# Kernel optimization log

Measured on AMD Instinct MI355X. Metric: run time of the kernel, lower is better.

## Reference

```python
import jax, jax.numpy as jnp
import numpy as np

BN_EPS = 1e-5
LN_EPS = 1e-5

N_NODES = 50000
N_EDGES = 800000
D_IN = 128
D_HID = 512


def _batchnorm(h, gamma, beta):
    # training-mode BatchNorm1d: biased variance over the node/batch dim
    m = jnp.mean(h, axis=0)
    v = jnp.mean(jnp.square(h - m), axis=0)
    return (h - m) * jax.lax.rsqrt(v + BN_EPS) * gamma + beta


def setup_inputs() -> dict:
    key = jax.random.key(0)
    ks = jax.random.split(key, 8)
    x = jax.random.normal(ks[0], (N_NODES, D_IN), dtype=jnp.float32)
    edge_index = jax.random.randint(ks[1], (2, N_EDGES), 0, N_NODES, dtype=jnp.int64)
    s1 = 1.0 / np.sqrt(D_IN)
    s2 = 1.0 / np.sqrt(D_HID)
    W1 = jax.random.uniform(ks[2], (D_IN, D_HID), jnp.float32, -s1, s1)
    b1 = jax.random.uniform(ks[3], (D_HID,), jnp.float32, -s1, s1)
    W2 = jax.random.uniform(ks[4], (D_HID, D_IN), jnp.float32, -s2, s2)
    b2 = jax.random.uniform(ks[5], (D_IN,), jnp.float32, -s2, s2)
    return {
        "x": x,
        "edge_index": edge_index,
        "W1": W1, "b1": b1,
        "bn1_g": jnp.ones((D_HID,), jnp.float32), "bn1_b": jnp.zeros((D_HID,), jnp.float32),
        "W2": W2, "b2": b2,
        "bn2_g": jnp.ones((D_IN,), jnp.float32), "bn2_b": jnp.zeros((D_IN,), jnp.float32),
        "ln_g": jnp.ones((D_IN,), jnp.float32), "ln_b": jnp.zeros((D_IN,), jnp.float32),
    }


def reference(x, edge_index, W1, b1, bn1_g, bn1_b, W2, b2, bn2_g, bn2_b, ln_g, ln_b):
    n = x.shape[0]
    src = edge_index[0]
    dst = edge_index[1]
    # GIN aggregation: sum of neighbor (source) features at each destination node
    agg = jax.ops.segment_sum(x[src], dst, num_segments=n)  # [N, D_IN]
    h = x + agg  # (1 + eps) * x + agg, eps = 0
    # MLP: Linear -> BN -> ReLU -> Linear -> BN -> ReLU (final activation)
    h = jax.nn.relu(_batchnorm(h @ W1 + b1, bn1_g, bn1_b))  # [N, D_HID]
    h = jax.nn.relu(_batchnorm(h @ W2 + b2, bn2_g, bn2_b))  # [N, D_IN]
    # residual + LayerNorm (dropout p=0 -> identity)
    out = h + x
    m = jnp.mean(out, axis=-1, keepdims=True)
    v = jnp.mean(jnp.square(out - m), axis=-1, keepdims=True)
    out = (out - m) * jax.lax.rsqrt(v + LN_EPS) * ln_g + ln_b
    return out
```

## Files before the change

kernel.cpp:

```cpp
#include <hip/hip_runtime.h>
#include <stdint.h>

#define N_NODES 50000
#define N_EDGES 800000
#define D_IN    128
#define D_HID   512
#define NPAD    50048
#define NTILES  391
#define SCAN_NB 196
#define G_TILES 782
#define G_BLOCKS 256
#define H1_FULL_NEED 64797440LL
#define FILL_CH 2048
#define FILL_SUB ((N_EDGES + FILL_CH - 1) / FILL_CH)

typedef __attribute__((ext_vector_type(8))) short short8;
typedef __attribute__((ext_vector_type(4))) float f32x4;

__device__ __forceinline__ float bf2f(unsigned short u) {
    union { unsigned int i; float f; } v; v.i = ((unsigned int)u) << 16; return v.f;
}
__device__ __forceinline__ unsigned short f2bf(float f) {
    union { float f; unsigned int i; } v; v.f = f;
    unsigned int r = v.i + 0x7fffu + ((v.i >> 16) & 1u);
    return (unsigned short)(r >> 16);
}
__device__ __forceinline__ float loadP(const void* p, long i, int isf) {
    return isf ? ((const float*)p)[i] : bf2f(((const unsigned short*)p)[i]);
}

__global__ void k_init(const void* __restrict__ x, const int* __restrict__ ei,
                       float* __restrict__ stats, int* __restrict__ counts,
                       int* __restrict__ flags) {
    int t = threadIdx.x;
    if (blockIdx.x < 201) {
        int i = blockIdx.x * 256 + t;
        if (i < 1408) stats[i] = 0.f;
        else if (i < 1408 + N_NODES) counts[i - 1408] = 0;
    } else {
        __shared__ int sh[2];
        if (t == 0) { sh[0] = 0; sh[1] = 1; }
        __syncthreads();
        const unsigned short* xu = (const unsigned short*)x;
        for (int i = t; i < 8192; i += 256)
            if (((xu[i] >> 7) & 0xFF) == 0xFF) sh[0] = 1;
        for (int k = t; k < 64; k += 256)
            if (ei[2 * k + 1] != 0) sh[1] = 0;
        __syncthreads();
        if (t == 0) { flags[0] = sh[0]; flags[1] = sh[1]; }
    }
}

__global__ void k_transpose2(const void* __restrict__ W1, const void* __restrict__ W2,
                             unsigned short* __restrict__ w1t, unsigned short* __restrict__ w2t,
                             const int* __restrict__ flags) {
    int isf = flags[0];
    int idx = blockIdx.x * 256 + threadIdx.x;
    if (idx < D_IN * D_HID) {
        int n = idx >> 7, k = idx & 127;
        int src = k * D_HID + n;
        w1t[idx] = isf ? f2bf(((const float*)W1)[src])
                       : ((const unsigned short*)W1)[src];
    } else {
        int j = idx - D_IN * D_HID;
        int n = j >> 9, k = j & 511;
        int src = k * D_IN + n;
        w2t[j] = isf ? f2bf(((const float*)W2)[src])
                     : ((const unsigned short*)W2)[src];
    }
}

__global__ __launch_bounds__(256) void k_count(const int* __restrict__ ei, int* __restrict__ counts,
                                               const int* __restrict__ flags) {
    int i64 = flags[1];
    int gid = blockIdx.x & 7;
    int sub = blockIdx.x >> 3;
    int lo = gid * (N_NODES / 8), hi = lo + (N_NODES / 8);
    int base = sub * FILL_CH + threadIdx.x;
#pragma unroll
    for (int i = 0; i < 8; i++) {
        int e = base + i * 256;
        if (e < N_EDGES) {
            int d = i64 ? ei[2 * N_EDGES + 2 * e] : ei[N_EDGES + e];
            d = min(max(d, 0), N_NODES - 1);
            if (d >= lo && d < hi) atomicAdd(&counts[d], 1);
        }
    }
}

__global__ __launch_bounds__(256) void k_scan_block(const int* __restrict__ counts,
                                                    int* __restrict__ rowptr,
                                                    int* __restrict__ partials) {
    __shared__ int a[256], b[256];
    int t = threadIdx.x;
    int idx = blockIdx.x * 256 + t;
    int c = (idx < N_NODES) ? counts[idx] : 0;
    a[t] = c;
    __syncthreads();
    int* src = a; int* dst = b;
    for (int off = 1; off < 256; off <<= 1) {
        dst[t] = src[t] + ((t >= off) ? src[t - off] : 0);
        __syncthreads();
        int* tmp = src; src = dst; dst = tmp;
    }
    if (idx < N_NODES) rowptr[idx] = src[t] - c;
    if (t == 255) partials[blockIdx.x] = src[255];
}

__global__ __launch_bounds__(256) void k_scan_add(int* __restrict__ rowptr, int* __restrict__ cursor,
                                                  const int* __restrict__ partials) {
    __shared__ int red[256];
    int t = threadIdx.x, bid = blockIdx.x;
    red[t] = (t < SCAN_NB && t < bid) ? partials[t] : 0;
    __syncthreads();
#pragma unroll
    for (int off = 128; off > 0; off >>= 1) {
        if (t < off) red[t] += red[t + off];
        __syncthreads();
    }
    int prefix = red[0];
    int idx = bid * 256 + t;
    if (idx < N_NODES) {
        int v = rowptr[idx] + prefix;
        rowptr[idx] = v;
        cursor[idx] = v;
    } else if (idx == N_NODES) {
        rowptr[N_NODES] = N_EDGES;
    }
}

__global__ __launch_bounds__(256) void k_fill(const int* __restrict__ ei, int* __restrict__ cursor,
                                              int* __restrict__ bucket, const int* __restrict__ flags) {
    int i64 = flags[1];
    int gid = blockIdx.x & 7;
    int sub = blockIdx.x >> 3;
    int lo = gid * (N_NODES / 8), hi = lo + (N_NODES / 8);
    int base = sub * FILL_CH + threadIdx.x;
#pragma unroll
    for (int i = 0; i < 8; i++) {
        int e = base + i * 256;
        if (e < N_EDGES) {
            int d = i64 ? ei[2 * N_EDGES + 2 * e] : ei[N_EDGES + e];
            d = min(max(d, 0), N_NODES - 1);
            if (d >= lo && d < hi) {
                int s = i64 ? ei[2 * e] : ei[e];
                s = min(max(s, 0), N_NODES - 1);
                int pos = atomicAdd(&cursor[d], 1);
                bucket[pos] = s;
            }
        }
    }
}

__global__ __launch_bounds__(256) void k_gather(const int* __restrict__ rowptr,
                                                const int* __restrict__ bucket,
                                                const void* __restrict__ x,
                                                unsigned short* __restrict__ agg,
                                                const int* __restrict__ flags) {
    int isf = flags[0];
    int w = threadIdx.x >> 6, lane = threadIdx.x & 63;
    int row = blockIdx.x * 4 + w;
    float a0 = 0.f, a1 = 0.f;
    if (row < N_NODES) {
        int beg = rowptr[row], end = rowptr[row + 1];
        if (isf) {
            const float* xf = (const float*)x;
            float2 v = *(const float2*)(xf + (size_t)row * D_IN + lane * 2);
            a0 = v.x; a1 = v.y;
            int j = beg;
            for (; j + 8 <= end; j += 8) {
                float2 n0 = *(const float2*)(xf + (size_t)bucket[j] * D_IN + lane * 2);
                float2 n1 = *(const float2*)(xf + (size_t)bucket[j + 1] * D_IN + lane * 2);
                float2 n2 = *(const float2*)(xf + (size_t)bucket[j + 2] * D_IN + lane * 2);
                float2 n3 = *(const float2*)(xf + (size_t)bucket[j + 3] * D_IN + lane * 2);
                float2 n4 = *(const float2*)(xf + (size_t)bucket[j + 4] * D_IN + lane * 2);
                float2 n5 = *(const float2*)(xf + (size_t)bucket[j + 5] * D_IN + lane * 2);
                float2 n6 = *(const float2*)(xf + (size_t)bucket[j + 6] * D_IN + lane * 2);
                float2 n7 = *(const float2*)(xf + (size_t)bucket[j + 7] * D_IN + lane * 2);
                a0 += ((n0.x + n1.x) + (n2.x + n3.x)) + ((n4.x + n5.x) + (n6.x + n7.x));
                a1 += ((n0.y + n1.y) + (n2.y + n3.y)) + ((n4.y + n5.y) + (n6.y + n7.y));
            }
            for (; j + 4 <= end; j += 4) {
                float2 n0 = *(const float2*)(xf + (size_t)bucket[j] * D_IN + lane * 2);
                float2 n1 = *(const float2*)(xf + (size_t)bucket[j + 1] * D_IN + lane * 2);
                float2 n2 = *(const float2*)(xf + (size_t)bucket[j + 2] * D_IN + lane * 2);
                float2 n3 = *(const float2*)(xf + (size_t)bucket[j + 3] * D_IN + lane * 2);
                a0 += (n0.x + n1.x) + (n2.x + n3.x);
                a1 += (n0.y + n1.y) + (n2.y + n3.y);
            }
            for (; j < end; j++) {
                float2 n = *(const float2*)(xf + (size_t)bucket[j] * D_IN + lane * 2);
                a0 += n.x; a1 += n.y;
            }
        } else {
            const unsigned int* xu = (const unsigned int*)x;
            unsigned int u = xu[(size_t)row * 64 + lane];
            a0 = bf2f(u & 0xffff); a1 = bf2f(u >> 16);
            int j = beg;
            for (; j + 8 <= end; j += 8) {
                unsigned int u0 = xu[(size_t)bucket[j] * 64 + lane];
                unsigned int u1 = xu[(size_t)bucket[j + 1] * 64 + lane];
                unsigned int u2 = xu[(size_t)bucket[j + 2] * 64 + lane];
                unsigned int u3 = xu[(size_t)bucket[j + 3] * 64 + lane];
                unsigned int u4 = xu[(size_t)bucket[j + 4] * 64 + lane];
                unsigned int u5 = xu[(size_t)bucket[j + 5] * 64 + lane];
                unsigned int u6 = xu[(size_t)bucket[j + 6] * 64 + lane];
                unsigned int u7 = xu[(size_t)bucket[j + 7] * 64 + lane];
                a0 += ((bf2f(u0 & 0xffff) + bf2f(u1 & 0xffff)) + (bf2f(u2 & 0xffff) + bf2f(u3 & 0xffff)))
                    + ((bf2f(u4 & 0xffff) + bf2f(u5 & 0xffff)) + (bf2f(u6 & 0xffff) + bf2f(u7 & 0xffff)));
                a1 += ((bf2f(u0 >> 16) + bf2f(u1 >> 16)) + (bf2f(u2 >> 16) + bf2f(u3 >> 16)))
                    + ((bf2f(u4 >> 16) + bf2f(u5 >> 16)) + (bf2f(u6 >> 16) + bf2f(u7 >> 16)));
            }
            for (; j + 4 <= end; j += 4) {
                unsigned int u0 = xu[(size_t)bucket[j] * 64 + lane];
                unsigned int u1 = xu[(size_t)bucket[j + 1] * 64 + lane];
                unsigned int u2 = xu[(size_t)bucket[j + 2] * 64 + lane];
                unsigned int u3 = xu[(size_t)bucket[j + 3] * 64 + lane];
                a0 += (bf2f(u0 & 0xffff) + bf2f(u1 & 0xffff)) + (bf2f(u2 & 0xffff) + bf2f(u3 & 0xffff));
                a1 += (bf2f(u0 >> 16) + bf2f(u1 >> 16)) + (bf2f(u2 >> 16) + bf2f(u3 >> 16));
            }
            for (; j < end; j++) {
                unsigned int n = xu[(size_t)bucket[j] * 64 + lane];
                a0 += bf2f(n & 0xffff); a1 += bf2f(n >> 16);
            }
        }
    }
    unsigned int o = (unsigned int)f2bf(a0) | ((unsigned int)f2bf(a1) << 16);
    ((unsigned int*)agg)[(size_t)row * 64 + lane] = o;
}

__global__ __launch_bounds__(256) void k_gram(const unsigned short* __restrict__ aggb,
                                              float* __restrict__ Gpart,
                                              float* __restrict__ colsum) {
    __shared__ unsigned short ldsT[128 * 64];
    int t = threadIdx.x;
    int wid = t >> 6, lane = t & 63;
    int wm = wid & 1, wn = wid >> 1;
    int quad = lane >> 4, l16 = lane & 15;
    f32x4 acc[4][4] = {};
    float cs = 0.f;
    int cscol = t & 127, cskh = t >> 7;
    for (int tile = blockIdx.x; tile < G_TILES; tile += G_BLOCKS) {
        __syncthreads();
        size_t rowbase = (size_t)tile * 64;
#pragma unroll
        for (int jj = 0; jj < 2; jj++) {
            int j = t + jj * 256;
            int c = j >> 5, rp = j & 31;
            uint4 v0 = *(const uint4*)(aggb + (rowbase + 2 * rp) * 128 + c * 8);
            uint4 v1 = *(const uint4*)(aggb + (rowbase + 2 * rp + 1) * 128 + c * 8);
            const unsigned short* p0 = (const unsigned short*)&v0;
            const unsigned short* p1 = (const unsigned short*)&v1;
            int k = 2 * rp, kc = k >> 3, ko = k & 7;
#pragma unroll
            for (int e = 0; e < 8; e++) {
                int col = c * 8 + e;
                *(unsigned int*)(ldsT + col * 64 + ((kc ^ (col & 7)) * 8) + ko) =
                    (unsigned int)p0[e] | ((unsigned int)p1[e] << 16);
            }
        }
        __syncthreads();
#pragma unroll
        for (int ksub = 0; ksub < 2; ksub++) {
            short8 fa[4], fb[4];
#pragma unroll
            for (int mt = 0; mt < 4; mt++) {
                int col = wm * 64 + mt * 16 + l16;
                fa[mt] = *(const short8*)(ldsT + col * 64 + (((ksub * 4 + quad) ^ (col & 7)) * 8));
            }
#pragma unroll
            for (int nt = 0; nt < 4; nt++) {
                int col = wn * 64 + nt * 16 + l16;
                fb[nt] = *(const short8*)(ldsT + col * 64 + (((ksub * 4 + quad) ^ (col & 7)) * 8));
            }
#pragma unroll
            for (int mt = 0; mt < 4; mt++)
#pragma unroll
                for (int nt = 0; nt < 4; nt++)
                    acc[mt][nt] = __builtin_amdgcn_mfma_f32_16x16x32_bf16(fa[mt], fb[nt], acc[mt][nt], 0, 0, 0);
        }
#pragma unroll
        for (int kc = 0; kc < 4; kc++) {
            short8 v = *(const short8*)(ldsT + cscol * 64 + (((cskh * 4 + kc) ^ (cscol & 7)) * 8));
#pragma unroll
            for (int e = 0; e < 8; e++) cs += bf2f((unsigned short)v[e]);
        }
    }
    float* gp = Gpart + (size_t)blockIdx.x * 16384;
#pragma unroll
    for (int mt = 0; mt < 4; mt++)
#pragma unroll
        for (int nt = 0; nt < 4; nt++) {
            int m = wm * 64 + mt * 16 + quad * 4;
            int n = wn * 64 + nt * 16 + l16;
#pragma unroll
            for (int rg = 0; rg < 4; rg++)
                gp[(m + rg) * 128 + n] = acc[mt][nt][rg];
        }
    atomicAdd(&colsum[cscol], cs);
}

__global__ void k_gred(const float* __restrict__ Gpart, float* __restrict__ G) {
    int i = blockIdx.x * 256 + threadIdx.x;
    float s = 0.f;
#pragma unroll 8
    for (int b = 0; b < G_BLOCKS; b++) s += Gpart[(size_t)b * 16384 + i];
    G[i] = s;
}

__global__ __launch_bounds__(256) void k_bn1(const float* __restrict__ G,
                                             const float* __restrict__ colsum,
                                             const unsigned short* __restrict__ w1t,
                                             const void* __restrict__ b1,
                                             float* __restrict__ sum1,
                                             float* __restrict__ sumsq1,
                                             const int* __restrict__ flags) {
    int isf = flags[0];
    __shared__ float wsh[4][128];
    int t = threadIdx.x, wid = t >> 6, lane = t & 63;
    int n = blockIdx.x * 4 + wid;
    unsigned int u = *(const unsigned int*)(w1t + (size_t)n * 128 + lane * 2);
    wsh[wid][lane * 2] = bf2f(u & 0xffff);
    wsh[wid][lane * 2 + 1] = bf2f(u >> 16);
    __syncthreads();
    const float* w = wsh[wid];
    const f32x4* g0 = (const f32x4*)(G + (size_t)lane * 128);
    const f32x4* g1 = (const f32x4*)(G + (size_t)(lane + 64) * 128);
    float t0 = 0.f, t1 = 0.f;
#pragma unroll 4
    for (int q4 = 0; q4 < 32; q4++) {
        f32x4 a = g0[q4], b = g1[q4];
        float w0 = w[q4 * 4], w1 = w[q4 * 4 + 1], w2 = w[q4 * 4 + 2], w3 = w[q4 * 4 + 3];
        t0 += a[0] * w0 + a[1] * w1 + a[2] * w2 + a[3] * w3;
        t1 += b[0] * w0 + b[1] * w1 + b[2] * w2 + b[3] * w3;
    }
    float sq = w[lane] * t0 + w[lane + 64] * t1;
    float s  = w[lane] * colsum[lane] + w[lane + 64] * colsum[lane + 64];
#pragma unroll
    for (int m = 1; m < 64; m <<= 1) {
        sq += __shfl_xor(sq, m, 64);
        s  += __shfl_xor(s, m, 64);
    }
    if (lane == 0) {
        float b = loadP(b1, n, isf);
        sum1[n]   = s + (float)N_NODES * b;
        sumsq1[n] = sq + 2.f * b * s + (float)N_NODES * b * b;
    }
}

__global__ __launch_bounds__(256, 2) void k_mlp1(const unsigned short* __restrict__ aggc,
                                                 const unsigned short* __restrict__ w1t,
                                                 const void* __restrict__ b1,
                                                 const void* __restrict__ g1,
                                                 const void* __restrict__ bb1,
                                                 const float* __restrict__ sum1,
                                                 const float* __restrict__ sumsq1,
                                                 unsigned short* __restrict__ h1c,
                                                 const int* __restrict__ flags) {
    __shared__ unsigned short bufA[128 * 128];
    __shared__ unsigned short bufW[128 * 128];
    int isf = flags[0];
    int t = threadIdx.x;
    int m0 = (blockIdx.x >> 2) * 128;
    int nb = blockIdx.x & 3;
    int r = t >> 1, half = t & 1;
    int wid = t >> 6, lane = t & 63;
    int wm = wid & 1, wn = wid >> 1;
    int quad = lane >> 4, l16 = lane & 15;
#pragma unroll
    for (int i = 0; i < 8; i++) {
        int chunk = half * 8 + i;
        int sw = ((chunk ^ (r & 15)) * 8);
        *(uint4*)(bufA + r * 128 + sw) = *(const uint4*)(aggc + (size_t)(m0 + r) * 128 + chunk * 8);
        *(uint4*)(bufW + r * 128 + sw) = *(const uint4*)(w1t + (size_t)(nb * 128 + r) * 128 + chunk * 8);
    }
    __syncthreads();
    f32x4 acc[4][4] = {};
#pragma unroll
    for (int ks = 0; ks < 4; ks++) {
        short8 af[4], bw[4];
#pragma unroll
        for (int mt = 0; mt < 4; mt++)
            af[mt] = *(const short8*)(bufA + (wm * 64 + mt * 16 + l16) * 128 + (((ks * 4 + quad) ^ l16) * 8));
#pragma unroll
        for (int nt = 0; nt < 4; nt++)
            bw[nt] = *(const short8*)(bufW + (wn * 64 + nt * 16 + l16) * 128 + (((ks * 4 + quad) ^ l16) * 8));
#pragma unroll
        for (int mt = 0; mt < 4; mt++)
#pragma unroll
            for (int nt = 0; nt < 4; nt++)
                acc[mt][nt] = __builtin_amdgcn_mfma_f32_16x16x32_bf16(af[mt], bw[nt], acc[mt][nt], 0, 0, 0);
    }
    __syncthreads();
#pragma unroll
    for (int nt = 0; nt < 4; nt++) {
        int nl = wn * 64 + nt * 16 + l16;
        int n1 = nb * 128 + nl;
        float mz = sum1[n1] * (1.f / N_NODES);
        float vz = sumsq1[n1] * (1.f / N_NODES) - mz * mz;
        float inv = rsqrtf(fmaxf(vz, 0.f) + 1e-5f);
        float A = loadP(g1, n1, isf) * inv;
        float C = loadP(bb1, n1, isf) - mz * A + loadP(b1, n1, isf) * A;
        int ccw = nl >> 3, cl = nl & 7;
#pragma unroll
        for (int mt = 0; mt < 4; mt++)
#pragma unroll
            for (int rg = 0; rg < 4; rg++) {
                int R = wm * 64 + mt * 16 + quad * 4 + rg;
                bufA[R * 128 + ((ccw ^ (R & 15)) * 8) + cl] = f2bf(fmaxf(acc[mt][nt][rg] * A + C, 0.f));
            }
    }
    __syncthreads();
#pragma unroll
    for (int i = 0; i < 8; i++) {
        int idx = t + i * 256;
        int rr = idx >> 4, chunk = idx & 15;
        *(uint4*)(h1c + (size_t)(m0 + rr) * D_HID + nb * 128 + chunk * 8) =
            *(const uint4*)(bufA + rr * 128 + ((chunk ^ (rr & 15)) * 8));
    }
}

__global__ __launch_bounds__(256, 2) void k_mlp1r(const unsigned short* __restrict__ aggb,
                                                  const unsigned short* __restrict__ w1t,
                                                  const void* __restrict__ b1,
                                                  unsigned short* __restrict__ h1,
                                                  float* __restrict__ sum1,
                                                  float* __restrict__ sumsq1,
                                                  const int* __restrict__ flags) {
    __shared__ unsigned short bufA[128 * 128];
    __shared__ unsigned short bufW[128 * 128];
    __shared__ float sred[256];
    int isf = flags[0];
    int t = threadIdx.x;
    int m0 = (blockIdx.x >> 2) * 128;
    int nb = blockIdx.x & 3;
    int r = t >> 1, half = t & 1;
    int wid = t >> 6, lane = t & 63;
    int wm = wid & 1, wn = wid >> 1;
    int quad = lane >> 4, l16 = lane & 15;
    sred[t] = 0.f;
#pragma unroll
    for (int i = 0; i < 8; i++) {
        int chunk = half * 8 + i;
        int sw = ((chunk ^ (r & 15)) * 8);
        *(uint4*)(bufA + r * 128 + sw) = *(const uint4*)(aggb + (size_t)(m0 + r) * 128 + chunk * 8);
        *(uint4*)(bufW + r * 128 + sw) = *(const uint4*)(w1t + (size_t)(nb * 128 + r) * 128 + chunk * 8);
    }
    __syncthreads();
    f32x4 acc[4][4] = {};
#pragma unroll
    for (int ks = 0; ks < 4; ks++) {
        short8 af[4], bw[4];
#pragma unroll
        for (int mt = 0; mt < 4; mt++)
            af[mt] = *(const short8*)(bufA + (wm * 64 + mt * 16 + l16) * 128 + (((ks * 4 + quad) ^ l16) * 8));
#pragma unroll
        for (int nt = 0; nt < 4; nt++)
            bw[nt] = *(const short8*)(bufW + (wn * 64 + nt * 16 + l16) * 128 + (((ks * 4 + quad) ^ l16) * 8));
#pragma unroll
        for (int mt = 0; mt < 4; mt++)
#pragma unroll
            for (int nt = 0; nt < 4; nt++)
                acc[mt][nt] = __builtin_amdgcn_mfma_f32_16x16x32_bf16(af[mt], bw[nt], acc[mt][nt], 0, 0, 0);
    }
    __syncthreads();
#pragma unroll
    for (int nt = 0; nt < 4; nt++) {
        int nl = wn * 64 + nt * 16 + l16;
        int n1 = nb * 128 + nl;
        float bias = loadP(b1, n1, isf);
        int ccw = nl >> 3, cl = nl & 7;
        float s = 0.f, ss = 0.f;
#pragma unroll
        for (int mt = 0; mt < 4; mt++)
#pragma unroll
            for (int rg = 0; rg < 4; rg++) {
                int R = wm * 64 + mt * 16 + quad * 4 + rg;
                float z = acc[mt][nt][rg] + bias;
                bufA[R * 128 + ((ccw ^ (R & 15)) * 8) + cl] = f2bf(z);
                if (m0 + R < N_NODES) { s += z; ss += z * z; }
            }
        s += __shfl_xor(s, 16, 64); ss += __shfl_xor(ss, 16, 64);
        s += __shfl_xor(s, 32, 64); ss += __shfl_xor(ss, 32, 64);
        if (quad == 0) { atomicAdd(&sred[nl], s); atomicAdd(&sred[128 + nl], ss); }
    }
    __syncthreads();
#pragma unroll
    for (int i = 0; i < 8; i++) {
        int idx = t + i * 256;
        int rr = idx >> 4, chunk = idx & 15;
        *(uint4*)(h1 + (size_t)(m0 + rr) * D_HID + nb * 128 + chunk * 8) =
            *(const uint4*)(bufA + rr * 128 + ((chunk ^ (rr & 15)) * 8));
    }
    if (t < 128)      atomicAdd(&sum1[nb * 128 + t], sred[t]);
    else              atomicAdd(&sumsq1[nb * 128 + (t - 128)], sred[t]);
}

__global__ __launch_bounds__(256, 3) void k_mlp2(const unsigned short* __restrict__ h1c,
                                                 const unsigned short* __restrict__ w2t,
                                                 const void* __restrict__ b2,
                                                 unsigned short* __restrict__ h2c,
                                                 float* __restrict__ sum2,
                                                 float* __restrict__ sumsq2,
                                                 const int* __restrict__ flags,
                                                 int roff) {
    __shared__ unsigned short bufA[64 * 128];
    __shared__ unsigned short bufW[128 * 128];
    __shared__ float sred[256];
    int isf = flags[0];
    int t = threadIdx.x;
    int m0 = blockIdx.x * 64;
    int rw = t >> 1, halfw = t & 1;
    int wid = t >> 6, lane = t & 63;
    int wm = wid & 1, wn = wid >> 1;
    int quad = lane >> 4, l16 = lane & 15;
    sred[t] = 0.f;
    f32x4 acc[2][4] = {};
    for (int kb = 0; kb < 4; kb++) {
        __syncthreads();
#pragma unroll
        for (int i = 0; i < 4; i++) {
            int idx = t + i * 256;
            int rr = idx >> 4, chunk = idx & 15;
            *(uint4*)(bufA + rr * 128 + ((chunk ^ (rr & 15)) * 8)) =
                *(const uint4*)(h1c + (size_t)(m0 + rr) * D_HID + kb * 128 + chunk * 8);
        }
#pragma unroll
        for (int i = 0; i < 8; i++) {
            int chunk = halfw * 8 + i;
            *(uint4*)(bufW + rw * 128 + ((chunk ^ (rw & 15)) * 8)) =
                *(const uint4*)(w2t + (size_t)rw * D_HID + kb * 128 + chunk * 8);
        }
        __syncthreads();
#pragma unroll
        for (int ks = 0; ks < 4; ks++) {
            short8 af[2], bw[4];
#pragma unroll
            for (int mt = 0; mt < 2; mt++)
                af[mt] = *(const short8*)(bufA + (wm * 32 + mt * 16 + l16) * 128 + (((ks * 4 + quad) ^ l16) * 8));
#pragma unroll
            for (int nt = 0; nt < 4; nt++)
                bw[nt] = *(const short8*)(bufW + (wn * 64 + nt * 16 + l16) * 128 + (((ks * 4 + quad) ^ l16) * 8));
#pragma unroll
            for (int mt = 0; mt < 2; mt++)
#pragma unroll
                for (int nt = 0; nt < 4; nt++)
                    acc[mt][nt] = __builtin_amdgcn_mfma_f32_16x16x32_bf16(af[mt], bw[nt], acc[mt][nt], 0, 0, 0);
        }
    }
    __syncthreads();
#pragma unroll
    for (int nt = 0; nt < 4; nt++) {
        int n = wn * 64 + nt * 16 + l16;
        float bias = loadP(b2, n, isf);
        float s = 0.f, ss = 0.f;
#pragma unroll
        for (int mt = 0; mt < 2; mt++) {
            int Rl = wm * 32 + mt * 16 + quad * 4;
#pragma unroll
            for (int rg = 0; rg < 4; rg++) {
                float z = acc[mt][nt][rg] + bias;
                bufW[(Rl + rg) * 128 + n] = f2bf(z);
                if (roff + m0 + Rl + rg < N_NODES) { s += z; ss += z * z; }
            }
        }
        s += __shfl_xor(s, 16, 64); ss += __shfl_xor(ss, 16, 64);
        s += __shfl_xor(s, 32, 64); ss += __shfl_xor(ss, 32, 64);
        if (quad == 0) { atomicAdd(&sred[n], s); atomicAdd(&sred[128 + n], ss); }
    }
    __syncthreads();
#pragma unroll
    for (int i = 0; i < 4; i++) {
        int idx = t + i * 256;
        int rr = idx >> 4, seg = idx & 15;
        *(uint4*)(h2c + (size_t)(m0 + rr) * D_IN + seg * 8) = *(const uint4*)(bufW + rr * 128 + seg * 8);
    }
    {
        int n = t & 127;
        if (t < 128) atomicAdd(&sum2[n], sred[n]);
        else         atomicAdd(&sumsq2[n], sred[128 + n]);
    }
}

__global__ __launch_bounds__(512, 4) void k_mlp2b(const unsigned short* __restrict__ h1,
                                                  const unsigned short* __restrict__ w2t,
                                                  const void* __restrict__ b2,
                                                  const void* __restrict__ g1,
                                                  const void* __restrict__ bb1,
                                                  const float* __restrict__ sum1,
                                                  const float* __restrict__ sumsq1,
                                                  unsigned short* __restrict__ h2,
                                                  float* __restrict__ sum2,
                                                  float* __restrict__ sumsq2,
                                                  const int* __restrict__ flags) {
    __shared__ unsigned short bufA[128 * 128];
    __shared__ unsigned short bufW[128 * 128];
    __shared__ float sred[256];
    __shared__ __align__(16) float bnA[512];
    __shared__ __align__(16) float bnC[512];
    int isf = flags[0];
    int t = threadIdx.x;
    int m0 = blockIdx.x * 128;
    int wid = t >> 6, lane = t & 63;
    int wm = wid & 3, wn = wid >> 2;
    int quad = lane >> 4, l16 = lane & 15;
    int chunkT = t & 15;
    if (t < 256) sred[t] = 0.f;
    if (t < 512) {
        float mz = sum1[t] * (1.f / N_NODES);
        float vz = sumsq1[t] * (1.f / N_NODES) - mz * mz;
        float inv = rsqrtf(fmaxf(vz, 0.f) + 1e-5f);
        float A = loadP(g1, t, isf) * inv;
        bnA[t] = A;
        bnC[t] = loadP(bb1, t, isf) - mz * A;
    }
    f32x4 acc[2][4] = {};
    for (int kb = 0; kb < 4; kb++) {
        __syncthreads();
        f32x4 A0 = *(const f32x4*)(bnA + kb * 128 + chunkT * 8);
        f32x4 A1 = *(const f32x4*)(bnA + kb * 128 + chunkT * 8 + 4);
        f32x4 C0 = *(const f32x4*)(bnC + kb * 128 + chunkT * 8);
        f32x4 C1 = *(const f32x4*)(bnC + kb * 128 + chunkT * 8 + 4);
#pragma unroll
        for (int i = 0; i < 4; i++) {
            int idx = t + i * 512;
            int rr = idx >> 4;
            uint4 v = *(const uint4*)(h1 + (size_t)(m0 + rr) * D_HID + kb * 128 + chunkT * 8);
            const unsigned short* pv = (const unsigned short*)&v;
            unsigned short o[8];
            o[0] = f2bf(fmaxf(bf2f(pv[0]) * A0[0] + C0[0], 0.f));
            o[1] = f2bf(fmaxf(bf2f(pv[1]) * A0[1] + C0[1], 0.f));
            o[2] = f2bf(fmaxf(bf2f(pv[2]) * A0[2] + C0[2], 0.f));
            o[3] = f2bf(fmaxf(bf2f(pv[3]) * A0[3] + C0[3], 0.f));
            o[4] = f2bf(fmaxf(bf2f(pv[4]) * A1[0] + C1[0], 0.f));
            o[5] = f2bf(fmaxf(bf2f(pv[5]) * A1[1] + C1[1], 0.f));
            o[6] = f2bf(fmaxf(bf2f(pv[6]) * A1[2] + C1[2], 0.f));
            o[7] = f2bf(fmaxf(bf2f(pv[7]) * A1[3] + C1[3], 0.f));
            *(uint4*)(bufA + rr * 128 + ((chunkT ^ (rr & 15)) * 8)) = *(const uint4*)o;
        }
#pragma unroll
        for (int i = 0; i < 4; i++) {
            int idx = t + i * 512;
            int rr = idx >> 4;
            *(uint4*)(bufW + rr * 128 + ((chunkT ^ (rr & 15)) * 8)) =
                *(const uint4*)(w2t + (size_t)rr * D_HID + kb * 128 + chunkT * 8);
        }
        __syncthreads();
#pragma unroll
        for (int ks = 0; ks < 4; ks++) {
            short8 af[2], bw[4];
#pragma unroll
            for (int mt = 0; mt < 2; mt++)
                af[mt] = *(const short8*)(bufA + (wm * 32 + mt * 16 + l16) * 128 + (((ks * 4 + quad) ^ l16) * 8));
#pragma unroll
            for (int nt = 0; nt < 4; nt++)
                bw[nt] = *(const short8*)(bufW + (wn * 64 + nt * 16 + l16) * 128 + (((ks * 4 + quad) ^ l16) * 8));
#pragma unroll
            for (int mt = 0; mt < 2; mt++)
#pragma unroll
                for (int nt = 0; nt < 4; nt++)
                    acc[mt][nt] = __builtin_amdgcn_mfma_f32_16x16x32_bf16(af[mt], bw[nt], acc[mt][nt], 0, 0, 0);
        }
    }
    __syncthreads();
#pragma unroll
    for (int nt = 0; nt < 4; nt++) {
        int n = wn * 64 + nt * 16 + l16;
        float bias = loadP(b2, n, isf);
        float s = 0.f, ss = 0.f;
#pragma unroll
        for (int mt = 0; mt < 2; mt++) {
            int Rl = wm * 32 + mt * 16 + quad * 4;
#pragma unroll
            for (int rg = 0; rg < 4; rg++) {
                float z = acc[mt][nt][rg] + bias;
                bufW[(Rl + rg) * 128 + n] = f2bf(z);
                if (m0 + Rl + rg < N_NODES) { s += z; ss += z * z; }
            }
        }
        s += __shfl_xor(s, 16, 64); ss += __shfl_xor(ss, 16, 64);
        s += __shfl_xor(s, 32, 64); ss += __shfl_xor(ss, 32, 64);
        if (quad == 0) { atomicAdd(&sred[n], s); atomicAdd(&sred[128 + n], ss); }
    }
    __syncthreads();
#pragma unroll
    for (int i = 0; i < 4; i++) {
        int idx = t + i * 512;
        int rr = idx >> 4, seg = idx & 15;
        *(uint4*)(h2 + (size_t)(m0 + rr) * D_IN + seg * 8) = *(const uint4*)(bufW + rr * 128 + seg * 8);
    }
    if (t < 256) {
        int n = t & 127;
        if (t < 128) atomicAdd(&sum2[n], sred[n]);
        else         atomicAdd(&sumsq2[n], sred[128 + n]);
    }
}

__global__ __launch_bounds__(256) void k_final(const unsigned short* __restrict__ h2,
                                               const void* __restrict__ x,
                                               const float* __restrict__ sum2,
                                               const float* __restrict__ sumsq2,
                                               const void* __restrict__ g2,
                                               const void* __restrict__ bb2,
                                               const void* __restrict__ lng,
                                               const void* __restrict__ lnb,
                                               void* __restrict__ out,
                                               const int* __restrict__ flags) {
    int isf = flags[0];
    __shared__ float a2s[D_IN], c2s[D_IN];
    int t = threadIdx.x;
    if (t < D_IN) {
        float m = sum2[t] * (1.f / N_NODES);
        float v = sumsq2[t] * (1.f / N_NODES) - m * m;
        float inv = rsqrtf(fmaxf(v, 0.f) + 1e-5f);
        float a = loadP(g2, t, isf) * inv;
        a2s[t] = a;
        c2s[t] = loadP(bb2, t, isf) - m * a;
    }
    __syncthreads();
    int w = t >> 6, lane = t & 63;
    int row = blockIdx.x * 4 + w;
    if (row >= N_NODES) return;
    size_t base = (size_t)row * D_IN;
    int c0 = lane * 2, c1 = lane * 2 + 1;
    unsigned int hu = ((const unsigned int*)h2)[base / 2 + lane];
    float x0, x1;
    if (isf) {
        float2 xv = *((const float2*)x + base / 2 + lane);
        x0 = xv.x; x1 = xv.y;
    } else {
        unsigned int xu = ((const unsigned int*)x)[base / 2 + lane];
        x0 = bf2f(xu & 0xffff); x1 = bf2f(xu >> 16);
    }
    float o0 = fmaxf(a2s[c0] * bf2f(hu & 0xffff) + c2s[c0], 0.f) + x0;
    float o1 = fmaxf(a2s[c1] * bf2f(hu >> 16) + c2s[c1], 0.f) + x1;
    float s = o0 + o1, ss = o0 * o0 + o1 * o1;
#pragma unroll
    for (int m = 1; m < 64; m <<= 1) {
        s += __shfl_xor(s, m, 64);
        ss += __shfl_xor(ss, m, 64);
    }
    float mean = s * (1.f / D_IN);
    float var = ss * (1.f / D_IN) - mean * mean;
    float inv = rsqrtf(fmaxf(var, 0.f) + 1e-5f);
    float r0 = (o0 - mean) * inv * loadP(lng, c0, isf) + loadP(lnb, c0, isf);
    float r1 = (o1 - mean) * inv * loadP(lng, c1, isf) + loadP(lnb, c1, isf);
    if (isf) {
        *((float2*)out + base / 2 + lane) = make_float2(r0, r1);
    } else {
        ((unsigned int*)out)[base / 2 + lane] = (unsigned int)f2bf(r0) | ((unsigned int)f2bf(r1) << 16);
    }
}

extern "C" void kernel_launch(void* const* d_in, const int* in_sizes, int n_in,
                              void* d_out, int out_size, void* d_ws, size_t ws_size,
                              hipStream_t stream) {
    const void* x    = d_in[0];
    const int*  ei   = (const int*)d_in[1];
    const void* W1   = d_in[2];
    const void* b1   = d_in[3];
    const void* bn1g = d_in[4];
    const void* bn1b = d_in[5];
    const void* W2   = d_in[6];
    const void* b2   = d_in[7];
    const void* bn2g = d_in[8];
    const void* bn2b = d_in[9];
    const void* lng  = d_in[10];
    const void* lnb  = d_in[11];

    char* ws = (char*)d_ws;
    float* stats   = (float*)ws;
    float* sum1    = stats;
    float* sumsq1  = stats + 512;
    float* sum2    = stats + 1024;
    float* sumsq2  = stats + 1152;
    float* colsum  = stats + 1280;
    int*   flags   = (int*)(ws + 5632);
    int*   partials= (int*)(ws + 5696);
    int*   rowptr  = (int*)(ws + 8192);
    int*   cursor  = (int*)(ws + 208256);
    unsigned short* w1t = (unsigned short*)(ws + 408320);
    unsigned short* w2t = (unsigned short*)(ws + 539392);
    float* G       = (float*)(ws + 670464);
    unsigned short* agg = (unsigned short*)(ws + 736000);
    unsigned short* h2  = agg;
    int*   bucket  = (int*)(ws + 13548288);
    float* Gpart   = (float*)(ws + 16748288);
    unsigned short* h1r = (unsigned short*)(ws + 13548288);

    k_init<<<202, 256, 0, stream>>>(x, ei, stats, cursor, flags);
    k_transpose2<<<512, 256, 0, stream>>>(W1, W2, w1t, w2t, flags);
    k_count<<<8 * FILL_SUB, 256, 0, stream>>>(ei, cursor, flags);
    k_scan_block<<<SCAN_NB, 256, 0, stream>>>(cursor, rowptr, partials);
    k_scan_add<<<SCAN_NB, 256, 0, stream>>>(rowptr, cursor, partials);
    k_fill<<<8 * FILL_SUB, 256, 0, stream>>>(ei, cursor, bucket, flags);
    k_gather<<<NPAD / 4, 256, 0, stream>>>(rowptr, bucket, x, agg, flags);

    if ((long long)ws_size >= H1_FULL_NEED) {
        k_mlp1r<<<NTILES * 4, 256, 0, stream>>>(agg, w1t, b1, h1r, sum1, sumsq1, flags);
        k_mlp2b<<<NTILES, 512, 0, stream>>>(h1r, w2t, b2, bn1g, bn1b, sum1, sumsq1,
                                            h2, sum2, sumsq2, flags);
    } else {
        k_gram<<<G_BLOCKS, 256, 0, stream>>>(agg, Gpart, colsum);
        k_gred<<<64, 256, 0, stream>>>(Gpart, G);
        k_bn1<<<128, 256, 0, stream>>>(G, colsum, w1t, b1, sum1, sumsq1, flags);
        long long avail = (long long)ws_size - 13548288LL;
        int max_tiles = (avail > 0) ? (int)(avail / 131072LL) : 1;
        if (max_tiles < 1)  max_tiles = 1;
        if (max_tiles > NTILES) max_tiles = NTILES;
        int nch = (NTILES + max_tiles - 1) / max_tiles;
        int per = (NTILES + nch - 1) / nch;
        for (int done = 0; done < NTILES; done += per) {
            int nt = NTILES - done;
            if (nt > per) nt = per;
            const unsigned short* aggc = agg + (size_t)done * 128 * 128;
            unsigned short* h2c = h2 + (size_t)done * 128 * 128;
            k_mlp1<<<nt * 4, 256, 0, stream>>>(aggc, w1t, b1, bn1g, bn1b, sum1, sumsq1, h1r, flags);
            k_mlp2<<<nt * 2, 256, 0, stream>>>(h1r, w2t, b2, h2c, sum2, sumsq2, flags, done * 128);
        }
    }

    k_final<<<(N_NODES + 3) / 4, 256, 0, stream>>>(h2, x, sum2, sumsq2, bn2g, bn2b, lng, lnb, d_out, flags);
}
```

Baseline: 323.4 us.

## Fuse weight transpose with edge counting and phase gather by source range

The weight-transpose and destination-count kernels become one launch with block ranges split between them, which saves one launch. The neighbor gather now passes over each row's bucket 8 times, loading only the sources that fall in the current node-range phase. The goal is to make concurrent waves touch the same slice of x at the same time and so improve L2 locality. The cost is rereading the bucket indices 8 times, extra branches, and loss of the independent unrolled loads that provided memory-level parallelism.

```diff
diff --git a/kernel.cpp b/kernel.cpp
--- a/kernel.cpp
+++ b/kernel.cpp
@@ -13,6 +13,7 @@
 #define H1_FULL_NEED 64797440LL
 #define FILL_CH 2048
 #define FILL_SUB ((N_EDGES + FILL_CH - 1) / FILL_CH)
+#define NPH 8
 
 typedef __attribute__((ext_vector_type(8))) short short8;
 typedef __attribute__((ext_vector_type(4))) float f32x4;
@@ -51,39 +52,40 @@
     }
 }
 
-__global__ void k_transpose2(const void* __restrict__ W1, const void* __restrict__ W2,
-                             unsigned short* __restrict__ w1t, unsigned short* __restrict__ w2t,
-                             const int* __restrict__ flags) {
+__global__ __launch_bounds__(256) void k_prep(const void* __restrict__ W1, const void* __restrict__ W2,
+                                              unsigned short* __restrict__ w1t, unsigned short* __restrict__ w2t,
+                                              const int* __restrict__ ei, int* __restrict__ counts,
+                                              const int* __restrict__ flags) {
     int isf = flags[0];
-    int idx = blockIdx.x * 256 + threadIdx.x;
-    if (idx < D_IN * D_HID) {
-        int n = idx >> 7, k = idx & 127;
-        int src = k * D_HID + n;
-        w1t[idx] = isf ? f2bf(((const float*)W1)[src])
-                       : ((const unsigned short*)W1)[src];
+    if (blockIdx.x < 512) {
+        int idx = blockIdx.x * 256 + threadIdx.x;
+        if (idx < D_IN * D_HID) {
+            int n = idx >> 7, k = idx & 127;
+            int src = k * D_HID + n;
+            w1t[idx] = isf ? f2bf(((const float*)W1)[src])
+                           : ((const unsigned short*)W1)[src];
+        } else {
+            int j = idx - D_IN * D_HID;
+            int n = j >> 9, k = j & 511;
+            int src = k * D_IN + n;
+            w2t[j] = isf ? f2bf(((const float*)W2)[src])
+                         : ((const unsigned short*)W2)[src];
+        }
     } else {
-        int j = idx - D_IN * D_HID;
-        int n = j >> 9, k = j & 511;
-        int src = k * D_IN + n;
-        w2t[j] = isf ? f2bf(((const float*)W2)[src])
-                     : ((const unsigned short*)W2)[src];
-    }
-}
-
-__global__ __launch_bounds__(256) void k_count(const int* __restrict__ ei, int* __restrict__ counts,
-                                               const int* __restrict__ flags) {
-    int i64 = flags[1];
-    int gid = blockIdx.x & 7;
-    int sub = blockIdx.x >> 3;
-    int lo = gid * (N_NODES / 8), hi = lo + (N_NODES / 8);
-    int base = sub * FILL_CH + threadIdx.x;
-#pragma unroll
-    for (int i = 0; i < 8; i++) {
-        int e = base + i * 256;
-        if (e < N_EDGES) {
-            int d = i64 ? ei[2 * N_EDGES + 2 * e] : ei[N_EDGES + e];
-            d = min(max(d, 0), N_NODES - 1);
-            if (d >= lo && d < hi) atomicAdd(&counts[d], 1);
+        int i64 = flags[1];
+        int bid = blockIdx.x - 512;
+        int gid = bid & 7;
+        int sub = bid >> 3;
+        int lo = gid * (N_NODES / 8), hi = lo + (N_NODES / 8);
+        int base = sub * FILL_CH + threadIdx.x;
+#pragma unroll
+        for (int i = 0; i < 8; i++) {
+            int e = base + i * 256;
+            if (e < N_EDGES) {
+                int d = i64 ? ei[2 * N_EDGES + 2 * e] : ei[N_EDGES + e];
+                d = min(max(d, 0), N_NODES - 1);
+                if (d >= lo && d < hi) atomicAdd(&counts[d], 1);
+            }
         }
     }
 }
@@ -167,61 +169,39 @@
             const float* xf = (const float*)x;
             float2 v = *(const float2*)(xf + (size_t)row * D_IN + lane * 2);
             a0 = v.x; a1 = v.y;
-            int j = beg;
-            for (; j + 8 <= end; j += 8) {
-                float2 n0 = *(const float2*)(xf + (size_t)bucket[j] * D_IN + lane * 2);
-                float2 n1 = *(const float2*)(xf + (size_t)bucket[j + 1] * D_IN + lane * 2);
-                float2 n2 = *(const float2*)(xf + (size_t)bucket[j + 2] * D_IN + lane * 2);
-                float2 n3 = *(const float2*)(xf + (size_t)bucket[j + 3] * D_IN + lane * 2);
-                float2 n4 = *(const float2*)(xf + (size_t)bucket[j + 4] * D_IN + lane * 2);
-                float2 n5 = *(const float2*)(xf + (size_t)bucket[j + 5] * D_IN + lane * 2);
-                float2 n6 = *(const float2*)(xf + (size_t)bucket[j + 6] * D_IN + lane * 2);
-                float2 n7 = *(const float2*)(xf + (size_t)bucket[j + 7] * D_IN + lane * 2);
-                a0 += ((n0.x + n1.x) + (n2.x + n3.x)) + ((n4.x + n5.x) + (n6.x + n7.x));
-                a1 += ((n0.y + n1.y) + (n2.y + n3.y)) + ((n4.y + n5.y) + (n6.y + n7.y));
-            }
-            for (; j + 4 <= end; j += 4) {
-                float2 n0 = *(const float2*)(xf + (size_t)bucket[j] * D_IN + lane * 2);
-                float2 n1 = *(const float2*)(xf + (size_t)bucket[j + 1] * D_IN + lane * 2);
-                float2 n2 = *(const float2*)(xf + (size_t)bucket[j + 2] * D_IN + lane * 2);
-                float2 n3 = *(const float2*)(xf + (size_t)bucket[j + 3] * D_IN + lane * 2);
-                a0 += (n0.x + n1.x) + (n2.x + n3.x);
-                a1 += (n0.y + n1.y) + (n2.y + n3.y);
-            }
-            for (; j < end; j++) {
-                float2 n = *(const float2*)(xf + (size_t)bucket[j] * D_IN + lane * 2);
-                a0 += n.x; a1 += n.y;
+            for (int p = 0; p < NPH; p++) {
+                int lo = p * (N_NODES / NPH), hi = lo + (N_NODES / NPH);
+                int j = beg;
+                for (; j + 4 <= end; j += 4) {
+                    int s0 = bucket[j], s1 = bucket[j + 1], s2 = bucket[j + 2], s3 = bucket[j + 3];
+                    if (s0 >= lo && s0 < hi) { float2 n = *(const float2*)(xf + (size_t)s0 * D_IN + lane * 2); a0 += n.x; a1 += n.y; }
+                    if (s1 >= lo && s1 < hi) { float2 n = *(const float2*)(xf + (size_t)s1 * D_IN + lane * 2); a0 += n.x; a1 += n.y; }
+                    if (s2 >= lo && s2 < hi) { float2 n = *(const float2*)(xf + (size_t)s2 * D_IN + lane * 2); a0 += n.x; a1 += n.y; }
+                    if (s3 >= lo && s3 < hi) { float2 n = *(const float2*)(xf + (size_t)s3 * D_IN + lane * 2); a0 += n.x; a1 += n.y; }
+                }
+                for (; j < end; j++) {
+                    int s = bucket[j];
+                    if (s >= lo && s < hi) { float2 n = *(const float2*)(xf + (size_t)s * D_IN + lane * 2); a0 += n.x; a1 += n.y; }
+                }
             }
         } else {
             const unsigned int* xu = (const unsigned int*)x;
             unsigned int u = xu[(size_t)row * 64 + lane];
             a0 = bf2f(u & 0xffff); a1 = bf2f(u >> 16);
-            int j = beg;
-            for (; j + 8 <= end; j += 8) {
-                unsigned int u0 = xu[(size_t)bucket[j] * 64 + lane];
-                unsigned int u1 = xu[(size_t)bucket[j + 1] * 64 + lane];
-                unsigned int u2 = xu[(size_t)bucket[j + 2] * 64 + lane];
-                unsigned int u3 = xu[(size_t)bucket[j + 3] * 64 + lane];
-                unsigned int u4 = xu[(size_t)bucket[j + 4] * 64 + lane];
-                unsigned int u5 = xu[(size_t)bucket[j + 5] * 64 + lane];
-                unsigned int u6 = xu[(size_t)bucket[j + 6] * 64 + lane];
-                unsigned int u7 = xu[(size_t)bucket[j + 7] * 64 + lane];
-                a0 += ((bf2f(u0 & 0xffff) + bf2f(u1 & 0xffff)) + (bf2f(u2 & 0xffff) + bf2f(u3 & 0xffff)))
-                    + ((bf2f(u4 & 0xffff) + bf2f(u5 & 0xffff)) + (bf2f(u6 & 0xffff) + bf2f(u7 & 0xffff)));
-                a1 += ((bf2f(u0 >> 16) + bf2f(u1 >> 16)) + (bf2f(u2 >> 16) + bf2f(u3 >> 16)))
-                    + ((bf2f(u4 >> 16) + bf2f(u5 >> 16)) + (bf2f(u6 >> 16) + bf2f(u7 >> 16)));
-            }
-            for (; j + 4 <= end; j += 4) {
-                unsigned int u0 = xu[(size_t)bucket[j] * 64 + lane];
-                unsigned int u1 = xu[(size_t)bucket[j + 1] * 64 + lane];
-                unsigned int u2 = xu[(size_t)bucket[j + 2] * 64 + lane];
-                unsigned int u3 = xu[(size_t)bucket[j + 3] * 64 + lane];
-                a0 += (bf2f(u0 & 0xffff) + bf2f(u1 & 0xffff)) + (bf2f(u2 & 0xffff) + bf2f(u3 & 0xffff));
-                a1 += (bf2f(u0 >> 16) + bf2f(u1 >> 16)) + (bf2f(u2 >> 16) + bf2f(u3 >> 16));
-            }
-            for (; j < end; j++) {
-                unsigned int n = xu[(size_t)bucket[j] * 64 + lane];
-                a0 += bf2f(n & 0xffff); a1 += bf2f(n >> 16);
+            for (int p = 0; p < NPH; p++) {
+                int lo = p * (N_NODES / NPH), hi = lo + (N_NODES / NPH);
+                int j = beg;
+                for (; j + 4 <= end; j += 4) {
+                    int s0 = bucket[j], s1 = bucket[j + 1], s2 = bucket[j + 2], s3 = bucket[j + 3];
+                    if (s0 >= lo && s0 < hi) { unsigned int n = xu[(size_t)s0 * 64 + lane]; a0 += bf2f(n & 0xffff); a1 += bf2f(n >> 16); }
+                    if (s1 >= lo && s1 < hi) { unsigned int n = xu[(size_t)s1 * 64 + lane]; a0 += bf2f(n & 0xffff); a1 += bf2f(n >> 16); }
+                    if (s2 >= lo && s2 < hi) { unsigned int n = xu[(size_t)s2 * 64 + lane]; a0 += bf2f(n & 0xffff); a1 += bf2f(n >> 16); }
+                    if (s3 >= lo && s3 < hi) { unsigned int n = xu[(size_t)s3 * 64 + lane]; a0 += bf2f(n & 0xffff); a1 += bf2f(n >> 16); }
+                }
+                for (; j < end; j++) {
+                    int s = bucket[j];
+                    if (s >= lo && s < hi) { unsigned int n = xu[(size_t)s * 64 + lane]; a0 += bf2f(n & 0xffff); a1 += bf2f(n >> 16); }
+                }
             }
         }
     }
@@ -789,8 +769,7 @@
     unsigned short* h1r = (unsigned short*)(ws + 13548288);
 
     k_init<<<202, 256, 0, stream>>>(x, ei, stats, cursor, flags);
-    k_transpose2<<<512, 256, 0, stream>>>(W1, W2, w1t, w2t, flags);
-    k_count<<<8 * FILL_SUB, 256, 0, stream>>>(ei, cursor, flags);
+    k_prep<<<512 + 8 * FILL_SUB, 256, 0, stream>>>(W1, W2, w1t, w2t, ei, cursor, flags);
     k_scan_block<<<SCAN_NB, 256, 0, stream>>>(cursor, rowptr, partials);
     k_scan_add<<<SCAN_NB, 256, 0, stream>>>(rowptr, cursor, partials);
     k_fill<<<8 * FILL_SUB, 256, 0, stream>>>(ei, cursor, bucket, flags);
```

Result: slower. 429.6 us (+32.8%).
